# Performance work log

Hardware: AMD Instinct MI355X
Metric: run time of the kernel (lower is better)

## Reference

```python
import jax, jax.numpy as jnp
import numpy as np

B, N, C = 32, 4096, 256
WS, SHIFT, H = 64, 32, 8
HD = C // H
NW = N // WS
HID = 4 * C
SCALE = HD ** -0.5
EPS = 1e-5


def _build_attn_mask():
    # canonical Swin 1D shift mask: 0 within same region, -100 across
    idx = np.zeros(N, dtype=np.int32)
    cnt = 0
    for sl in (slice(0, N - WS), slice(N - WS, N - SHIFT), slice(N - SHIFT, N)):
        idx[sl] = cnt
        cnt += 1
    win = idx.reshape(NW, WS)
    diff = win[:, None, :] - win[:, :, None]
    return jnp.asarray(np.where(diff != 0, -100.0, 0.0).astype(np.float32))


def setup_inputs() -> dict:
    key = jax.random.key(0)
    ks = jax.random.split(key, 12)
    g = lambda i, shape, sc=0.02: jax.random.normal(ks[i], shape, jnp.float32) * sc
    return {
        "x": jax.random.normal(ks[0], (B, N, C), jnp.float32),
        "attn_mask": _build_attn_mask(),
        "norm1_w": jnp.ones((C,), jnp.float32),
        "norm1_b": jnp.zeros((C,), jnp.float32),
        "qkv_w": g(1, (3 * C, C)),
        "qkv_b": jnp.zeros((3 * C,), jnp.float32),
        "pos_w": g(2, (C, C, 3)),
        "pos_b": jnp.zeros((C,), jnp.float32),
        "proj_w": g(3, (C, C)),
        "proj_b": jnp.zeros((C,), jnp.float32),
        "norm2_w": jnp.ones((C,), jnp.float32),
        "norm2_b": jnp.zeros((C,), jnp.float32),
        "fc1_w": g(4, (HID, C)),
        "fc1_b": jnp.zeros((HID,), jnp.float32),
        "fc2_w": g(5, (C, HID)),
        "fc2_b": jnp.zeros((C,), jnp.float32),
    }


def _ln(x, w, b):
    m = x.mean(-1, keepdims=True)
    v = ((x - m) ** 2).mean(-1, keepdims=True)
    return (x - m) * jax.lax.rsqrt(v + EPS) * w + b


def reference(x, attn_mask, norm1_w, norm1_b, qkv_w, qkv_b, pos_w, pos_b,
              proj_w, proj_b, norm2_w, norm2_b, fc1_w, fc1_b, fc2_w, fc2_b):
    Bw = B * NW
    h = _ln(x, norm1_w, norm1_b)
    hs = jnp.roll(h, -SHIFT, axis=1)                      # cyclic shift
    xw = hs.reshape(Bw, WS, C)                            # window partition
    qkv = (xw @ qkv_w.T + qkv_b).reshape(Bw, WS, 3, H, HD)
    qkv = qkv.transpose(2, 0, 3, 1, 4)                    # [3, Bw, H, WS, HD]
    q, k, v = qkv[0] * SCALE, qkv[1], qkv[2]
    attn = jnp.einsum('bhqd,bhkd->bhqk', q, k)            # [Bw, H, WS, WS]
    attn = attn.reshape(B, NW, H, WS, WS) + attn_mask[None, :, None]
    attn = jax.nn.softmax(attn.reshape(Bw, H, WS, WS), axis=-1)
    # LePE: depthwise-style Conv1d over window axis, channels head-major
    vc = v.transpose(0, 1, 3, 2).reshape(Bw, C, WS)
    lepe = jax.lax.conv_general_dilated(
        vc, pos_w, window_strides=(1,), padding=((1, 1),),
        dimension_numbers=('NCH', 'OIH', 'NCH')) + pos_b[None, :, None]
    out = jnp.einsum('bhqk,bhkd->bhqd', attn, v)
    out = out.transpose(0, 2, 1, 3).reshape(Bw, WS, C) + lepe.transpose(0, 2, 1)
    out = out @ proj_w.T + proj_b
    out = out.reshape(B, N, C)                            # window reverse
    out = jnp.roll(out, SHIFT, axis=1)                    # reverse shift
    x1 = x + out
    h2 = _ln(x1, norm2_w, norm2_b)
    m = jax.nn.gelu(h2 @ fc1_w.T + fc1_b, approximate=False) @ fc2_w.T + fc2_b
    return x1 + m
```

## Files before the change

### kernel.cpp

```cpp
#include <hip/hip_runtime.h>

typedef unsigned short u16;
typedef unsigned int   u32;
typedef short bf16x8 __attribute__((ext_vector_type(8)));
typedef short bf16x4 __attribute__((ext_vector_type(4)));
typedef float f32x4  __attribute__((ext_vector_type(4)));

#define TT   131072
#define SCALE 0.17677669529663687f

__device__ __forceinline__ float bf2f(u32 u) {
    u32 v = u << 16;
    float f;
    __builtin_memcpy(&f, &v, 4);
    return f;
}
__device__ __forceinline__ u16 f2bf(float f) {
    u32 v;
    __builtin_memcpy(&v, &f, 4);
    u32 r = v + 0x7fffu + ((v >> 16) & 1u);
    return (u16)(r >> 16);
}

__device__ __forceinline__ u32 cvtpk(float a, float b) {
    u32 r;
    asm("v_cvt_pk_bf16_f32 %0, %1, %2" : "=v"(r) : "v"(a), "v"(b));
    return r;
}

#if __has_builtin(__builtin_amdgcn_mfma_f32_16x16x16bf16_1k)
#define HAVE_MFMA16_BUILTIN 1
#endif

__device__ __forceinline__ f32x4 mfma16(bf16x4 a, bf16x4 b, f32x4 c) {
#ifdef HAVE_MFMA16_BUILTIN
    return __builtin_amdgcn_mfma_f32_16x16x16bf16_1k(a, b, c, 0, 0, 0);
#else
    asm volatile("v_mfma_f32_16x16x16_bf16 %0, %1, %2, %0"
                 : "+v"(c) : "v"(a), "v"(b));
    return c;
#endif
}

#define GLD16(g, l)                                                           \
    __builtin_amdgcn_global_load_lds(                                         \
        (const __attribute__((address_space(1))) void*)(g),                   \
        (__attribute__((address_space(3))) void*)(l), 16, 0, 0)

__global__ __launch_bounds__(256) void cvt_kernel(
    const float* __restrict__ qkvw, const float* __restrict__ projw,
    const float* __restrict__ fc1w, const float* __restrict__ fc2w,
    u16* __restrict__ dst) {
    int i = blockIdx.x * 256 + threadIdx.x;
    if (i >= 983048) return;
    float v;
    if (i < 196608)       v = qkvw[i];
    else if (i < 458752)  v = fc1w[i - 196608];
    else if (i < 720896)  v = fc2w[i - 458752];
    else if (i < 983040) {
        int local = i - 720896;
        int kk = local & 1023;
        if (kk >= 256) return;
        v = projw[(local >> 10) * 256 + kk];
    } else v = 0.0f;
    dst[i] = f2bf(v);
}

__global__ __launch_bounds__(256) void compose_kernel(
    const float* __restrict__ projw, const float* __restrict__ posw,
    const float* __restrict__ projb, const float* __restrict__ posb,
    u16* __restrict__ pjl, float* __restrict__ bias2) {
    int c = blockIdx.x, t = threadIdx.x;
    __shared__ float pr[256];
    pr[t] = projw[c * 256 + t];
    __syncthreads();
    #pragma unroll
    for (int r = 0; r < 3; ++r) {
        int kp = r * 256 + t;
        int tap = kp >> 8, ci = kp & 255;
        float acc = 0.f;
        for (int j = 0; j < 256; ++j)
            acc += pr[j] * posw[j * 768 + ci * 3 + tap];
        pjl[(size_t)c * 1024 + 256 + kp] = f2bf(acc);
    }
    float b = pr[t] * posb[t];
    #pragma unroll
    for (int o = 32; o > 0; o >>= 1) b += __shfl_down(b, o);
    __shared__ float pb4[4];
    if ((t & 63) == 0) pb4[t >> 6] = b;
    __syncthreads();
    if (t == 0) bias2[c] = projb[c] + pb4[0] + pb4[1] + pb4[2] + pb4[3];
}

template <int SH>
__global__ __launch_bounds__(256) void ln_kernel(const float* __restrict__ x,
                                                 const float* __restrict__ w,
                                                 const float* __restrict__ bb,
                                                 u16* __restrict__ out) {
    int wid = threadIdx.x >> 6, lane = threadIdx.x & 63;
    int tl = blockIdx.x * 4 + wid;
    int src = (tl & ~4095) | ((tl + SH) & 4095);
    int c = lane * 4;
    float4 v = *(const float4*)(x + (size_t)src * 256 + c);
    float s1 = v.x + v.y + v.z + v.w;
    float s2 = v.x * v.x + v.y * v.y + v.z * v.z + v.w * v.w;
    #pragma unroll
    for (int o = 32; o > 0; o >>= 1) {
        s1 += __shfl_xor(s1, o);
        s2 += __shfl_xor(s2, o);
    }
    float mean = s1 * (1.0f / 256.0f);
    float rs = rsqrtf(s2 * (1.0f / 256.0f) - mean * mean + 1e-5f);
    float4 wv = *(const float4*)(w + c);
    float4 bv = *(const float4*)(bb + c);
    uint2 o2;
    o2.x = cvtpk((v.x - mean) * rs * wv.x + bv.x, (v.y - mean) * rs * wv.y + bv.y);
    o2.y = cvtpk((v.z - mean) * rs * wv.z + bv.z, (v.w - mean) * rs * wv.w + bv.w);
    *(uint2*)(out + (size_t)tl * 256 + c) = o2;
}

template <int MODE, int ACT, int AM>
__global__ __launch_bounds__(256) void mgemm(
    const u16* __restrict__ A, const u16* __restrict__ A2,
    const u16* __restrict__ W, const u16* __restrict__ Z,
    const float* __restrict__ bias, u16* __restrict__ Cb,
    float* __restrict__ Cf, const float* __restrict__ resf,
    int Nc, int K) {
    __shared__ u16 As[2][128 * 32];
    __shared__ u16 Bs[2][128 * 32];
    const int tid = threadIdx.x;
    const int m0 = blockIdx.x * 128, n0 = blockIdx.y * 128;
    const int w4 = tid >> 6, lane = tid & 63;
    const int srow = 32 * w4 + (lane >> 2);
    const int scol = (lane & 3) * 8;
    const u16* ag = (AM == 0) ? A + (size_t)(m0 + srow) * K + scol : A;
    const u16* bg = W + (size_t)(n0 + srow) * K + scol;
    const int lofs = w4 * 1024;
    const int frow = lane & 15, fk = (lane >> 4) * 8;
    const int am = (w4 & 1) * 64, bn = (w4 >> 1) * 64;

    const u16 *pA00, *pA10, *pA01, *pA11, *pA02, *pA12, *pA03, *pA13;
    u32 m0r1 = ~0u, m1r1 = ~0u, m0r3 = ~0u, m1r3 = ~0u;
    if constexpr (AM == 1) {
        int t0 = m0 + srow, t1 = t0 + 16;
        int tq0 = t0 & 63, tq1 = t1 & 63;
        pA00 = A + (size_t)t0 * 256 + scol;
        pA10 = A + (size_t)t1 * 256 + scol;
        pA01 = (tq0 > 0)  ? A2 + (long)(t0 - 1) * 768 + 512 + scol : Z;
        m0r1 = (tq0 > 0)  ? ~0u : 0u;
        pA11 = (tq1 > 0)  ? A2 + (long)(t1 - 1) * 768 + 512 + scol : Z;
        m1r1 = (tq1 > 0)  ? ~0u : 0u;
        pA02 = A2 + (size_t)t0 * 768 + 512 + scol;
        pA12 = A2 + (size_t)t1 * 768 + 512 + scol;
        pA03 = (tq0 < 63) ? A2 + (long)(t0 + 1) * 768 + 512 + scol : Z;
        m0r3 = (tq0 < 63) ? ~0u : 0u;
        pA13 = (tq1 < 63) ? A2 + (long)(t1 + 1) * 768 + 512 + scol : Z;
        m1r3 = (tq1 < 63) ? ~0u : 0u;
    }

    f32x4 acc[4][4];
    #pragma unroll
    for (int i = 0; i < 4; ++i)
        #pragma unroll
        for (int j = 0; j < 4; ++j) acc[i][j] = (f32x4){0.f, 0.f, 0.f, 0.f};

    auto STAGE = [&](int b, int k0) {
        u16* lA = &As[b][lofs];
        u16* lB = &Bs[b][lofs];
        if constexpr (AM == 1) {
            int kl = k0 & 255;
            const u16 *p0, *p1;
            u32 q0 = ~0u, q1 = ~0u;
            switch (k0 >> 8) {
                case 0:  p0 = pA00; p1 = pA10; break;
                case 1:  p0 = pA01; p1 = pA11; q0 = m0r1; q1 = m1r1; break;
                case 2:  p0 = pA02; p1 = pA12; break;
                default: p0 = pA03; p1 = pA13; q0 = m0r3; q1 = m1r3; break;
            }
            GLD16(p0 + (kl & q0), lA);
            GLD16(p1 + (kl & q1), lA + 512);
        } else {
            GLD16(ag + k0, lA);
            GLD16(ag + k0 + (size_t)16 * K, lA + 512);
        }
        GLD16(bg + k0, lB);
        GLD16(bg + (size_t)16 * K + k0, lB + 512);
    };
    auto COMPUTE = [&](int b) {
        bf16x8 af[4], bfr[4];
        #pragma unroll
        for (int mi = 0; mi < 4; ++mi)
            af[mi] = *(const bf16x8*)&As[b][(am + mi * 16 + frow) * 32 + fk];
        #pragma unroll
        for (int ni = 0; ni < 4; ++ni)
            bfr[ni] = *(const bf16x8*)&Bs[b][(bn + ni * 16 + frow) * 32 + fk];
        #pragma unroll
        for (int mi = 0; mi < 4; ++mi)
            #pragma unroll
            for (int ni = 0; ni < 4; ++ni)
                acc[mi][ni] = __builtin_amdgcn_mfma_f32_16x16x32_bf16(
                    af[mi], bfr[ni], acc[mi][ni], 0, 0, 0);
    };

    STAGE(0, 0);
    int cur = 0;
    const int nt = K >> 5;
    for (int t = 0; t < nt - 1; ++t) {
        STAGE(cur ^ 1, (t + 1) << 5);
        asm volatile("s_waitcnt vmcnt(4)" ::: "memory");
        __builtin_amdgcn_s_barrier();
        COMPUTE(cur);
        asm volatile("s_waitcnt lgkmcnt(0)" ::: "memory");
        __builtin_amdgcn_s_barrier();
        cur ^= 1;
    }
    asm volatile("s_waitcnt vmcnt(0)" ::: "memory");
    __builtin_amdgcn_s_barrier();
    COMPUTE(cur);

    const int erow = am + ((lane >> 4) << 2);
    const int ecol = bn + (lane & 15);
    #pragma unroll
    for (int ni = 0; ni < 4; ++ni) {
        int c = n0 + ecol + ni * 16;
        float bv = bias[c];
        #pragma unroll
        for (int mi = 0; mi < 4; ++mi) {
            #pragma unroll
            for (int reg = 0; reg < 4; ++reg) {
                int r = m0 + erow + mi * 16 + reg;
                float v = acc[mi][ni][reg] + bv;
                if (ACT == 1) v = 0.5f * v * (1.0f + erff(v * 0.70710678118654752f));
                if (MODE == 0) {
                    Cb[(size_t)r * Nc + c] = f2bf(v);
                } else if (MODE == 2) {
                    size_t drl = (size_t)((r & ~4095) | ((r + 32) & 4095));
                    Cf[drl * 256 + c] = v + resf[drl * 256 + c];
                } else {
                    Cf[(size_t)r * 256 + c] = v + resf[(size_t)r * 256 + c];
                }
            }
        }
    }
}

__global__ __launch_bounds__(256) void attn_mfma(const u16* __restrict__ qkv,
                                                 const float* __restrict__ mask,
                                                 u16* __restrict__ outb) {
    __shared__ u16 Vt[8][32][68];
    __shared__ float Mt[64][68];
    __shared__ int mflag;

    const int w   = blockIdx.x;
    const int nw  = w & 63;
    const int tid = threadIdx.x;
    const int wid = tid >> 6, lane = tid & 63;
    const int g = lane >> 4, q15 = lane & 15;

    if (tid == 0) mflag = 0;
    __syncthreads();

    {
        const float* mrow = mask + (size_t)nw * 4096;
        int nz = 0;
        #pragma unroll
        for (int i = 0; i < 16; ++i) {
            int e = i * 256 + tid;
            float m = mrow[e];
            nz |= (m != 0.0f);
            Mt[e & 63][e >> 6] = m;
        }
        if (nz) mflag = 1;
    }

    {
        const u16* vg = qkv + (size_t)(w * 64) * 768 + 512;
        #pragma unroll
        for (int p = 0; p < 8; ++p) {
            int t  = lane;
            int c0 = wid * 8 + p * 32;
            uint4 u = *(const uint4*)(vg + (size_t)t * 768 + c0);
            u16 el[8];
            *(uint4*)el = u;
            int h = c0 >> 5, d0 = c0 & 31;
            #pragma unroll
            for (int j = 0; j < 8; ++j) Vt[h][d0 + j][t] = el[j];
        }
    }
    __syncthreads();

    const int hasmask = mflag;

    #pragma unroll
    for (int hh = 0; hh < 2; ++hh) {
        const int h = wid * 2 + hh;

        const u16* kbase = qkv + (size_t)(w * 64) * 768 + 256 + h * 32 + g * 8;
        const u16* qbase = qkv + (size_t)(w * 64) * 768 +       h * 32 + g * 8;
        bf16x8 kf[4], qf[4];
        #pragma unroll
        for (int mt = 0; mt < 4; ++mt)
            kf[mt] = *(const bf16x8*)(kbase + (size_t)(16 * mt + q15) * 768);
        #pragma unroll
        for (int nt = 0; nt < 4; ++nt)
            qf[nt] = *(const bf16x8*)(qbase + (size_t)(16 * nt + q15) * 768);

        f32x4 s[4][4];
        #pragma unroll
        for (int mt = 0; mt < 4; ++mt)
            #pragma unroll
            for (int nt = 0; nt < 4; ++nt) s[mt][nt] = (f32x4){0.f, 0.f, 0.f, 0.f};
        #pragma unroll
        for (int mt = 0; mt < 4; ++mt)
            #pragma unroll
            for (int nt = 0; nt < 4; ++nt)
                s[mt][nt] = __builtin_amdgcn_mfma_f32_16x16x32_bf16(
                    kf[mt], qf[nt], s[mt][nt], 0, 0, 0);

        if (hasmask) {
            #pragma unroll
            for (int mt = 0; mt < 4; ++mt)
                #pragma unroll
                for (int nt = 0; nt < 4; ++nt)
                    #pragma unroll
                    for (int r = 0; r < 4; ++r)
                        s[mt][nt][r] = s[mt][nt][r] * SCALE +
                                       Mt[16 * mt + 4 * g + r][16 * nt + q15];
        } else {
            #pragma unroll
            for (int mt = 0; mt < 4; ++mt)
                #pragma unroll
                for (int nt = 0; nt < 4; ++nt)
                    #pragma unroll
                    for (int r = 0; r < 4; ++r)
                        s[mt][nt][r] *= SCALE;
        }

        float inv[4];
        #pragma unroll
        for (int nt = 0; nt < 4; ++nt) {
            float mx = -3.0e38f;
            #pragma unroll
            for (int mt = 0; mt < 4; ++mt)
                #pragma unroll
                for (int r = 0; r < 4; ++r) mx = fmaxf(mx, s[mt][nt][r]);
            mx = fmaxf(mx, __shfl_xor(mx, 16));
            mx = fmaxf(mx, __shfl_xor(mx, 32));
            float sum = 0.f;
            #pragma unroll
            for (int mt = 0; mt < 4; ++mt)
                #pragma unroll
                for (int r = 0; r < 4; ++r) {
                    float p = __expf(s[mt][nt][r] - mx);
                    s[mt][nt][r] = p;
                    sum += p;
                }
            sum += __shfl_xor(sum, 16);
            sum += __shfl_xor(sum, 32);
            inv[nt] = 1.0f / sum;
        }

        bf16x4 pb[4][4];
        #pragma unroll
        for (int mt = 0; mt < 4; ++mt)
            #pragma unroll
            for (int nt = 0; nt < 4; ++nt) {
                u32 pk[2];
                pk[0] = cvtpk(s[mt][nt][0], s[mt][nt][1]);
                pk[1] = cvtpk(s[mt][nt][2], s[mt][nt][3]);
                bf16x4 bv;
                __builtin_memcpy(&bv, pk, 8);
                pb[mt][nt] = bv;
            }

        f32x4 o[2][4];
        #pragma unroll
        for (int ma = 0; ma < 2; ++ma)
            #pragma unroll
            for (int nt = 0; nt < 4; ++nt) o[ma][nt] = (f32x4){0.f, 0.f, 0.f, 0.f};
        #pragma unroll
        for (int kt = 0; kt < 4; ++kt) {
            bf16x4 a0 = *(const bf16x4*)&Vt[h][q15][16 * kt + 4 * g];
            bf16x4 a1 = *(const bf16x4*)&Vt[h][16 + q15][16 * kt + 4 * g];
            #pragma unroll
            for (int nt = 0; nt < 4; ++nt) {
                o[0][nt] = mfma16(a0, pb[kt][nt], o[0][nt]);
                o[1][nt] = mfma16(a1, pb[kt][nt], o[1][nt]);
            }
        }

        u16* ob = outb + (size_t)(w * 64) * 256 + h * 32;
        #pragma unroll
        for (int nt = 0; nt < 4; ++nt) {
            float iv = inv[nt];
            int tok = 16 * nt + q15;
            #pragma unroll
            for (int ma = 0; ma < 2; ++ma) {
                uint2 val;
                val.x = cvtpk(o[ma][nt][0] * iv, o[ma][nt][1] * iv);
                val.y = cvtpk(o[ma][nt][2] * iv, o[ma][nt][3] * iv);
                *(uint2*)(ob + (size_t)tok * 256 + 16 * ma + 4 * g) = val;
            }
        }
    }
}

extern "C" void kernel_launch(void* const* d_in, const int* in_sizes, int n_in,
                              void* d_out, int out_size, void* d_ws, size_t ws_size,
                              hipStream_t stream) {
    const float* x     = (const float*)d_in[0];
    const float* mask  = (const float*)d_in[1];
    const float* n1w   = (const float*)d_in[2];
    const float* n1b   = (const float*)d_in[3];
    const float* qkvw  = (const float*)d_in[4];
    const float* qkvbi = (const float*)d_in[5];
    const float* posw  = (const float*)d_in[6];
    const float* posb  = (const float*)d_in[7];
    const float* projw = (const float*)d_in[8];
    const float* projb = (const float*)d_in[9];
    const float* n2w   = (const float*)d_in[10];
    const float* n2b   = (const float*)d_in[11];
    const float* fc1w  = (const float*)d_in[12];
    const float* fc1b  = (const float*)d_in[13];
    const float* fc2w  = (const float*)d_in[14];
    const float* fc2b  = (const float*)d_in[15];

    int CB = 32;
    while (CB > 1 && (size_t)CB * 4096 * 4096 + 1967120ull > ws_size) CB >>= 1;
    const int TC = CB * 4096;

    char* ws = (char*)d_ws;
    u16*   hs   = (u16*)ws;
    u16*   attn = (u16*)(ws + (size_t)TC * 512);
    float* x1   = (float*)(ws + (size_t)TC * 1024);
    u16*   qkv  = (u16*)(ws + (size_t)TC * 2048);
    u16*   mid  = qkv;
    u16*   wbf  = (u16*)(ws + (size_t)TC * 4096);
    u16* qkvw_b = wbf;
    u16* fc1w_b = wbf + 196608;
    u16* fc2w_b = wbf + 458752;
    u16* pjl    = wbf + 720896;
    u16* zero16 = wbf + 983040;
    float* bias2 = (float*)((char*)wbf + 1966096);

    cvt_kernel<<<3841, 256, 0, stream>>>(qkvw, projw, fc1w, fc2w, wbf);
    compose_kernel<<<256, 256, 0, stream>>>(projw, posw, projb, posb, pjl, bias2);

    for (int t0 = 0; t0 < TT; t0 += TC) {
        const float* xc = x + (size_t)t0 * 256;
        ln_kernel<32><<<TC / 4, 256, 0, stream>>>(xc, n1w, n1b, hs);
        mgemm<0, 0, 0><<<dim3(TC / 128, 6), 256, 0, stream>>>(
            hs, nullptr, qkvw_b, nullptr, qkvbi, qkv, nullptr, nullptr, 768, 256);
        attn_mfma<<<TC / 64, 256, 0, stream>>>(qkv, mask, attn);
        mgemm<2, 0, 1><<<dim3(TC / 128, 2), 256, 0, stream>>>(
            attn, qkv, pjl, zero16, bias2, nullptr, x1, xc, 256, 1024);
        ln_kernel<0><<<TC / 4, 256, 0, stream>>>(x1, n2w, n2b, hs);
        mgemm<0, 1, 0><<<dim3(TC / 128, 8), 256, 0, stream>>>(
            hs, nullptr, fc1w_b, nullptr, fc1b, mid, nullptr, nullptr, 1024, 256);
        mgemm<3, 0, 0><<<dim3(TC / 128, 2), 256, 0, stream>>>(
            mid, nullptr, fc2w_b, nullptr, fc2b, nullptr,
            (float*)d_out + (size_t)t0 * 256, x1, 256, 1024);
    }
}
```

Before: 1.026 ms.

## Pre-swizzle weights into MFMA fragment order and load B directly to registers

Weight conversion now writes qkv, fc1 and fc2 weights in a pre-shuffled layout matching the MFMA B-fragment order. A new dgemm kernel uses that layout to load B straight from global memory into registers, stages only A through LDS with a 3-buffer ring, and uses the 16x16x32 bf16 MFMA. The goal is to cut LDS traffic, LDS usage and barrier pressure so occupancy can rise. It also reworks zero-padding pointer selection in the attention-projection GEMM. The risk is that per-wave global B loads become uncoalesced or add latency, and the manual vmcnt waits must be exactly right.

```diff
diff --git a/kernel.cpp b/kernel.cpp
--- a/kernel.cpp
+++ b/kernel.cpp
@@ -54,10 +54,20 @@
     int i = blockIdx.x * 256 + threadIdx.x;
     if (i >= 983048) return;
     float v;
-    if (i < 196608)       v = qkvw[i];
-    else if (i < 458752)  v = fc1w[i - 196608];
-    else if (i < 720896)  v = fc2w[i - 458752];
-    else if (i < 983040) {
+    if (i < 720896) {
+        const float* W;
+        int e, K, ksmask, cbshift;
+        if (i < 196608)      { W = qkvw; e = i;          K = 256;  ksmask = 7;  cbshift = 6; }
+        else if (i < 458752) { W = fc1w; e = i - 196608; K = 256;  ksmask = 7;  cbshift = 6; }
+        else                 { W = fc2w; e = i - 458752; K = 1024; ksmask = 31; cbshift = 8; }
+        int f = e >> 9, l = (e >> 3) & 63, j = e & 7;
+        int nf = f & 7;
+        int ks = (f >> 3) & ksmask;
+        int cb = f >> cbshift;
+        int row = cb * 128 + nf * 16 + (l & 15);
+        int col = ks * 32 + ((l >> 4) << 3) + j;
+        v = W[row * K + col];
+    } else if (i < 983040) {
         int local = i - 720896;
         int kk = local & 1023;
         if (kk >= 256) return;
@@ -117,6 +127,107 @@
     o2.x = cvtpk((v.x - mean) * rs * wv.x + bv.x, (v.y - mean) * rs * wv.y + bv.y);
     o2.y = cvtpk((v.z - mean) * rs * wv.z + bv.z, (v.w - mean) * rs * wv.w + bv.w);
     *(uint2*)(out + (size_t)tl * 256 + c) = o2;
+}
+
+template <int MODE, int ACT>
+__global__ __launch_bounds__(256, 4) void dgemm(
+    const u16* __restrict__ A, const u16* __restrict__ Wsh,
+    const float* __restrict__ bias, u16* __restrict__ Cb,
+    float* __restrict__ Cf, const float* __restrict__ resf,
+    int Nc, int K) {
+    __shared__ u16 As[3][128 * 32];
+    const int tid = threadIdx.x;
+    const int m0 = blockIdx.x * 128;
+    const int w4 = tid >> 6, lane = tid & 63;
+    const int srow = 32 * w4 + (lane >> 2);
+    const int scol = (lane & 3) * 8;
+    const u16* ag  = A + (size_t)(m0 + srow) * K + scol;
+    const u16* ag2 = ag + (size_t)16 * K;
+    const int frow = lane & 15, fk = (lane >> 4) * 8;
+    const int am = (w4 & 1) * 64;
+    const int bn16 = (w4 >> 1) * 4;
+    const int KS = K >> 5;
+    const u16* wq = Wsh + ((size_t)blockIdx.y * KS * 8 + bn16) * 512 + lane * 8;
+    const int lofs = w4 * 1024;
+
+    f32x4 acc[4][4];
+    #pragma unroll
+    for (int i = 0; i < 4; ++i)
+        #pragma unroll
+        for (int j = 0; j < 4; ++j) acc[i][j] = (f32x4){0.f, 0.f, 0.f, 0.f};
+
+    bf16x8 R0[4], R1[4];
+    auto STAGE = [&](int b, int ks) {
+        GLD16(ag  + ks * 32, &As[b][lofs]);
+        GLD16(ag2 + ks * 32, &As[b][lofs + 512]);
+    };
+    auto LOADB = [&](bf16x8* R, int ks) {
+        const u16* p = wq + (size_t)ks * 4096;
+        #pragma unroll
+        for (int ni = 0; ni < 4; ++ni) R[ni] = *(const bf16x8*)(p + ni * 512);
+    };
+    auto COMPUTE = [&](int b, bf16x8* R) {
+        #pragma unroll
+        for (int mi = 0; mi < 4; ++mi) {
+            bf16x8 af = *(const bf16x8*)&As[b][(am + mi * 16 + frow) * 32 + fk];
+            #pragma unroll
+            for (int ni = 0; ni < 4; ++ni)
+                acc[mi][ni] = __builtin_amdgcn_mfma_f32_16x16x32_bf16(
+                    af, R[ni], acc[mi][ni], 0, 0, 0);
+        }
+    };
+
+    STAGE(0, 0);
+    STAGE(1, 1);
+    LOADB(R0, 0);
+    int bc = 0;
+    for (int t = 0; t + 2 < KS; t += 2) {
+        asm volatile("s_waitcnt vmcnt(6)" ::: "memory");
+        __builtin_amdgcn_s_barrier();
+        int bs = bc + 2; if (bs >= 3) bs -= 3;
+        STAGE(bs, t + 2);
+        LOADB(R1, t + 1);
+        COMPUTE(bc, R0);
+        bc = bc + 1; if (bc >= 3) bc -= 3;
+
+        asm volatile("s_waitcnt vmcnt(6)" ::: "memory");
+        __builtin_amdgcn_s_barrier();
+        if (t + 3 < KS) { int b2 = bc + 2; if (b2 >= 3) b2 -= 3; STAGE(b2, t + 3); }
+        LOADB(R0, t + 2);
+        COMPUTE(bc, R1);
+        bc = bc + 1; if (bc >= 3) bc -= 3;
+    }
+    asm volatile("s_waitcnt vmcnt(6)" ::: "memory");
+    __builtin_amdgcn_s_barrier();
+    LOADB(R1, KS - 1);
+    COMPUTE(bc, R0);
+    bc = bc + 1; if (bc >= 3) bc -= 3;
+    asm volatile("s_waitcnt vmcnt(4)" ::: "memory");
+    __builtin_amdgcn_s_barrier();
+    COMPUTE(bc, R1);
+
+    const int n0 = blockIdx.y * 128;
+    const int erow = am + ((lane >> 4) << 2);
+    const int ecol = (w4 >> 1) * 64 + (lane & 15);
+    #pragma unroll
+    for (int ni = 0; ni < 4; ++ni) {
+        int c = n0 + ecol + ni * 16;
+        float bv = bias[c];
+        #pragma unroll
+        for (int mi = 0; mi < 4; ++mi) {
+            #pragma unroll
+            for (int reg = 0; reg < 4; ++reg) {
+                int r = m0 + erow + mi * 16 + reg;
+                float v = acc[mi][ni][reg] + bv;
+                if (ACT == 1) v = 0.5f * v * (1.0f + erff(v * 0.70710678118654752f));
+                if (MODE == 0) {
+                    Cb[(size_t)r * Nc + c] = f2bf(v);
+                } else {
+                    Cf[(size_t)r * 256 + c] = v + resf[(size_t)r * 256 + c];
+                }
+            }
+        }
+    }
 }
 
 template <int MODE, int ACT, int AM>
@@ -140,22 +251,17 @@
     const int am = (w4 & 1) * 64, bn = (w4 >> 1) * 64;
 
     const u16 *pA00, *pA10, *pA01, *pA11, *pA02, *pA12, *pA03, *pA13;
-    u32 m0r1 = ~0u, m1r1 = ~0u, m0r3 = ~0u, m1r3 = ~0u;
     if constexpr (AM == 1) {
         int t0 = m0 + srow, t1 = t0 + 16;
         int tq0 = t0 & 63, tq1 = t1 & 63;
         pA00 = A + (size_t)t0 * 256 + scol;
         pA10 = A + (size_t)t1 * 256 + scol;
         pA01 = (tq0 > 0)  ? A2 + (long)(t0 - 1) * 768 + 512 + scol : Z;
-        m0r1 = (tq0 > 0)  ? ~0u : 0u;
         pA11 = (tq1 > 0)  ? A2 + (long)(t1 - 1) * 768 + 512 + scol : Z;
-        m1r1 = (tq1 > 0)  ? ~0u : 0u;
         pA02 = A2 + (size_t)t0 * 768 + 512 + scol;
         pA12 = A2 + (size_t)t1 * 768 + 512 + scol;
         pA03 = (tq0 < 63) ? A2 + (long)(t0 + 1) * 768 + 512 + scol : Z;
-        m0r3 = (tq0 < 63) ? ~0u : 0u;
         pA13 = (tq1 < 63) ? A2 + (long)(t1 + 1) * 768 + 512 + scol : Z;
-        m1r3 = (tq1 < 63) ? ~0u : 0u;
     }
 
     f32x4 acc[4][4];
@@ -170,15 +276,16 @@
         if constexpr (AM == 1) {
             int kl = k0 & 255;
             const u16 *p0, *p1;
-            u32 q0 = ~0u, q1 = ~0u;
             switch (k0 >> 8) {
-                case 0:  p0 = pA00; p1 = pA10; break;
-                case 1:  p0 = pA01; p1 = pA11; q0 = m0r1; q1 = m1r1; break;
-                case 2:  p0 = pA02; p1 = pA12; break;
-                default: p0 = pA03; p1 = pA13; q0 = m0r3; q1 = m1r3; break;
+                case 0:  p0 = pA00 + kl; p1 = pA10 + kl; break;
+                case 1:  p0 = (pA01 == Z) ? Z : pA01 + kl;
+                         p1 = (pA11 == Z) ? Z : pA11 + kl; break;
+                case 2:  p0 = pA02 + kl; p1 = pA12 + kl; break;
+                default: p0 = (pA03 == Z) ? Z : pA03 + kl;
+                         p1 = (pA13 == Z) ? Z : pA13 + kl; break;
             }
-            GLD16(p0 + (kl & q0), lA);
-            GLD16(p1 + (kl & q1), lA + 512);
+            GLD16(p0, lA);
+            GLD16(p1, lA + 512);
         } else {
             GLD16(ag + k0, lA);
             GLD16(ag + k0 + (size_t)16 * K, lA + 512);
@@ -436,9 +543,9 @@
     u16*   qkv  = (u16*)(ws + (size_t)TC * 2048);
     u16*   mid  = qkv;
     u16*   wbf  = (u16*)(ws + (size_t)TC * 4096);
-    u16* qkvw_b = wbf;
-    u16* fc1w_b = wbf + 196608;
-    u16* fc2w_b = wbf + 458752;
+    u16* qkv_sh = wbf;
+    u16* fc1_sh = wbf + 196608;
+    u16* fc2_sh = wbf + 458752;
     u16* pjl    = wbf + 720896;
     u16* zero16 = wbf + 983040;
     float* bias2 = (float*)((char*)wbf + 1966096);
@@ -449,16 +556,16 @@
     for (int t0 = 0; t0 < TT; t0 += TC) {
         const float* xc = x + (size_t)t0 * 256;
         ln_kernel<32><<<TC / 4, 256, 0, stream>>>(xc, n1w, n1b, hs);
-        mgemm<0, 0, 0><<<dim3(TC / 128, 6), 256, 0, stream>>>(
-            hs, nullptr, qkvw_b, nullptr, qkvbi, qkv, nullptr, nullptr, 768, 256);
+        dgemm<0, 0><<<dim3(TC / 128, 6), 256, 0, stream>>>(
+            hs, qkv_sh, qkvbi, qkv, nullptr, nullptr, 768, 256);
         attn_mfma<<<TC / 64, 256, 0, stream>>>(qkv, mask, attn);
         mgemm<2, 0, 1><<<dim3(TC / 128, 2), 256, 0, stream>>>(
             attn, qkv, pjl, zero16, bias2, nullptr, x1, xc, 256, 1024);
         ln_kernel<0><<<TC / 4, 256, 0, stream>>>(x1, n2w, n2b, hs);
-        mgemm<0, 1, 0><<<dim3(TC / 128, 8), 256, 0, stream>>>(
-            hs, nullptr, fc1w_b, nullptr, fc1b, mid, nullptr, nullptr, 1024, 256);
-        mgemm<3, 0, 0><<<dim3(TC / 128, 2), 256, 0, stream>>>(
-            mid, nullptr, fc2w_b, nullptr, fc2b, nullptr,
-            (float*)d_out + (size_t)t0 * 256, x1, 256, 1024);
-    }
-}
+        dgemm<0, 1><<<dim3(TC / 128, 8), 256, 0, stream>>>(
+            hs, fc1_sh, fc1b, mid, nullptr, nullptr, 1024, 256);
+        dgemm<3, 0><<<dim3(TC / 128, 2), 256, 0, stream>>>(
+            mid, fc2_sh, fc2b, nullptr, (float*)d_out + (size_t)t0 * 256, x1,
+            256, 1024);
+    }
+}
```

After: 1.051 ms. +2.4%, slower.
